# Kernel tuning notes

Hardware: AMD Instinct MI355X
Metric: run time of the kernel (lower is better)

## Reference

```python
import jax, jax.numpy as jnp
import numpy as np

N = 4096      # nodes
F = 512       # nfeat
D = 64        # nhid per head
H = 8         # nheads
C = 40        # nclass
ALPHA = 0.2   # leakyrelu slope
NEG = -1e9    # mask value (finite for bf16/fp16 safety; exp -> 0)
EDGE_P = 0.004


def setup_inputs() -> dict:
    key = jax.random.key(0)
    ks = jax.random.split(key, 8)
    x = jax.random.normal(ks[0], (N, F), jnp.float32)
    adj = jax.random.uniform(ks[1], (N, N)) < EDGE_P
    adj = adj | jnp.eye(N, dtype=bool)  # self-loops: every softmax row valid
    init = lambda k, shape, fan: jax.random.normal(k, shape, jnp.float32) / np.sqrt(fan)
    W1 = init(ks[2], (H, F, D), F)        # per-head tran.weight^T
    a1_src = init(ks[3], (H, D), D)       # att1 (j / source term)
    a1_dst = init(ks[4], (H, D), D)       # att2 (i / destination term)
    W2 = init(ks[5], (H * D, C), H * D)   # output head tran
    a2_src = init(ks[6], (C,), C)
    a2_dst = init(ks[7], (C,), C)
    return dict(x=x, adj=adj, W1=W1, a1_src=a1_src, a1_dst=a1_dst,
                W2=W2, a2_src=a2_src, a2_dst=a2_dst)


def reference(x, adj, W1, a1_src, a1_dst, W2, a2_src, a2_dst):
    # ---- layer 1: H heads in parallel (dropout = identity in eval) ----
    h = jnp.einsum('nf,hfd->hnd', x, W1)              # [H,N,D]
    si = jnp.einsum('hnd,hd->hn', h, a1_dst)          # att2(h): i term
    sj = jnp.einsum('hnd,hd->hn', h, a1_src)          # att1(h): j term
    e = jax.nn.leaky_relu(si[:, :, None] + sj[:, None, :], ALPHA)  # [H,N,N]
    e = jnp.where(adj[None], e, NEG)                  # mask non-edges
    p = jax.nn.softmax(e, axis=-1)                    # softmax over neighbors j
    out = jnp.einsum('hij,hjd->hid', p, h)            # [H,N,D]
    # torch.cat(heads, dim=1) -> [N, H*D] with heads contiguous
    x2 = jax.nn.elu(jnp.transpose(out, (1, 0, 2)).reshape(N, H * D))
    # ---- output attention head ----
    h2 = x2 @ W2                                      # [N,C]
    e2 = jax.nn.leaky_relu((h2 @ a2_dst)[:, None] + (h2 @ a2_src)[None, :], ALPHA)
    e2 = jnp.where(adj, e2, NEG)
    p2 = jax.nn.softmax(e2, axis=-1)
    return p2 @ h2                                    # [N,C]
```

## Files before the change

### kernel.cpp

```cpp
#include <hip/hip_runtime.h>

#define NN 4096
#define FF 512
#define DD 64
#define HH 8
#define CC 40
#define HD (HH * DD)
#define CP 64
#define MAXDEG 128
#define ALPHA 0.2f

#define L2BM 16
#define L2BK 32

typedef __attribute__((ext_vector_type(8))) short bf16x8;
typedef __attribute__((ext_vector_type(4))) float f32x4;

__device__ __forceinline__ float bf2f(unsigned short u) {
    union { unsigned int i; float f; } v;
    v.i = ((unsigned int)u) << 16;
    return v.f;
}

__device__ __forceinline__ unsigned short f2bf(float f) {
    union { float f; unsigned int u; } v;
    v.f = f;
    unsigned int r = v.u + 0x7fffu + ((v.u >> 16) & 1u);
    return (unsigned short)(r >> 16);
}

__device__ __forceinline__ float wave_sum(float v) {
    #pragma unroll
    for (int off = 32; off; off >>= 1) v += __shfl_xor(v, off, 64);
    return v;
}

__device__ __forceinline__ float wave_max(float v) {
    #pragma unroll
    for (int off = 32; off; off >>= 1) v = fmaxf(v, __shfl_xor(v, off, 64));
    return v;
}

__device__ __forceinline__ float read_f(const void* src, int i, int isBf16) {
    if (isBf16) return bf2f(((const unsigned short*)src)[i]);
    return ((const float*)src)[i];
}

__device__ __forceinline__ int sniff_x(const void* xraw, int tid, int* fS) {
    if (tid == 0) *fS = 1;
    __syncthreads();
    int bad = 0;
    const unsigned int* xw = (const unsigned int*)xraw;
    #pragma unroll
    for (int q = 0; q < 4; q++) {
        unsigned int w = xw[(tid & 255) * 4 + q];
        unsigned int e0 = (w >> 7) & 0xffu;
        unsigned int e1 = (w >> 23) & 0xffu;
        if (e0 >= 0x90u || e1 >= 0x90u) bad = 1;
    }
    if (bad) *fS = 0;
    __syncthreads();
    return *fS;
}

__global__ __launch_bounds__(256) void prep(const unsigned char* __restrict__ adj,
                                            const void* __restrict__ x,
                                            const void* __restrict__ W1,
                                            const void* __restrict__ W2,
                                            const void* __restrict__ a1s,
                                            const void* __restrict__ a1d,
                                            const void* __restrict__ a2s,
                                            const void* __restrict__ a2d,
                                            int* __restrict__ nbr,
                                            int* __restrict__ deg,
                                            unsigned short* __restrict__ W1bth,
                                            unsigned short* __restrict__ W1btl,
                                            float* __restrict__ W2p,
                                            float* __restrict__ a1sf,
                                            float* __restrict__ a1df,
                                            float* __restrict__ a2sf,
                                            float* __restrict__ a2df) {
    __shared__ int cnt;
    __shared__ int fS;
    int t = threadIdx.x;
    int blk = blockIdx.x;

    if (blk < NN) {
        if (t == 0) { cnt = 0; fS = 1; }
        __syncthreads();
        if (adj[(size_t)t * (NN + 1)] == 0) fS = 0;
        __syncthreads();
        int isByte = fS;
        int i = blk;
        if (isByte) {
            uint4 v = ((const uint4*)(adj + (size_t)i * NN))[t];
            unsigned int u[4] = { v.x, v.y, v.z, v.w };
            int base = t * 16;
            #pragma unroll
            for (int q = 0; q < 4; q++) {
                #pragma unroll
                for (int b = 0; b < 4; b++) {
                    if ((u[q] >> (8 * b)) & 0xffu) {
                        int p = atomicAdd(&cnt, 1);
                        if (p < MAXDEG) nbr[(size_t)i * MAXDEG + p] = base + q * 4 + b;
                    }
                }
            }
        } else {
            const int4* row = (const int4*)((const int*)adj + (size_t)i * NN);
            #pragma unroll
            for (int q = 0; q < 4; q++) {
                int idx4 = q * 256 + t;
                int4 v = row[idx4];
                int base = idx4 * 4;
                if (v.x) { int p = atomicAdd(&cnt, 1); if (p < MAXDEG) nbr[(size_t)i * MAXDEG + p] = base; }
                if (v.y) { int p = atomicAdd(&cnt, 1); if (p < MAXDEG) nbr[(size_t)i * MAXDEG + p] = base + 1; }
                if (v.z) { int p = atomicAdd(&cnt, 1); if (p < MAXDEG) nbr[(size_t)i * MAXDEG + p] = base + 2; }
                if (v.w) { int p = atomicAdd(&cnt, 1); if (p < MAXDEG) nbr[(size_t)i * MAXDEG + p] = base + 3; }
            }
        }
        __syncthreads();
        if (t == 0) deg[i] = min(cnt, MAXDEG);
        return;
    }

    int bf = sniff_x(x, t, &fS);

    if (blk < NN + 64) {
        int b = blk - NN;
        int ob = b * 4096 + t * 16;
        int row = ob >> 9;
        int f0 = ob & 511;
        int hd = row >> 6, d = row & 63;
        unsigned short hi[16], lo[16];
        #pragma unroll
        for (int q = 0; q < 16; q++) {
            float v = read_f(W1, (hd * FF + f0 + q) * DD + d, bf);
            unsigned short h16 = f2bf(v);
            hi[q] = h16;
            lo[q] = f2bf(v - bf2f(h16));
        }
        #pragma unroll
        for (int q = 0; q < 16; q++) {
            W1bth[(size_t)row * FF + f0 + q] = hi[q];
            W1btl[(size_t)row * FF + f0 + q] = lo[q];
        }
        return;
    }

    int i = (blk - NN - 64) * 256 + t;
    const int nW2p = HD * CP;
    const int nA1 = HD;
    if (i < nW2p) {
        int k = i / CP, c = i % CP;
        W2p[i] = (c < CC) ? read_f(W2, k * CC + c, bf) : 0.f;
        return;
    }
    i -= nW2p;
    if (i < nA1) { a1sf[i] = read_f(a1s, i, bf); return; }
    i -= nA1;
    if (i < nA1) { a1df[i] = read_f(a1d, i, bf); return; }
    i -= nA1;
    if (i < CC) { a2sf[i] = read_f(a2s, i, bf); return; }
    i -= CC;
    if (i < CC) { a2df[i] = read_f(a2d, i, bf); return; }
}

__global__ __launch_bounds__(256) void l1_gemm(const void* __restrict__ xraw,
                                               const unsigned short* __restrict__ W1bth,
                                               const unsigned short* __restrict__ W1btl,
                                               const float* __restrict__ a1sf,
                                               const float* __restrict__ a1df,
                                               unsigned short* __restrict__ hb,
                                               float* __restrict__ si,
                                               float* __restrict__ sj) {
    __shared__ __align__(16) unsigned short Ah[64][40];
    __shared__ __align__(16) unsigned short Al[64][40];
    __shared__ __align__(16) unsigned short Bh[64][40];
    __shared__ __align__(16) unsigned short Bl[64][40];
    __shared__ int fS;

    int bm = blockIdx.x, hd = blockIdx.y;
    int tid = threadIdx.x;
    int isBf16 = sniff_x(xraw, tid, &fS);

    int wave = tid >> 6, lane = tid & 63;
    int wm = wave >> 1, wn = wave & 1;
    int lr = lane & 15, lg = lane >> 4;
    int srow = tid >> 2;
    int sseg = (tid & 3) * 8;

    const unsigned short* wAp = W1bth + (size_t)(hd * 64 + srow) * FF + sseg;
    const unsigned short* wBp = W1btl + (size_t)(hd * 64 + srow) * FF + sseg;

    f32x4 acc[2][2];
    #pragma unroll
    for (int r = 0; r < 2; r++)
        #pragma unroll
        for (int c = 0; c < 2; c++) acc[r][c] = (f32x4){0.f, 0.f, 0.f, 0.f};

    if (isBf16) {
        const unsigned short* xp = (const unsigned short*)xraw
                                 + (size_t)(bm * 64 + srow) * FF + sseg;
        uint4 ra = *(const uint4*)xp;
        uint4 rb = *(const uint4*)wAp;
        for (int kk = 0; kk < FF; kk += 32) {
            __syncthreads();
            *(uint4*)&Ah[srow][sseg] = ra;
            *(uint4*)&Bh[srow][sseg] = rb;
            __syncthreads();
            int kn = (kk + 32 < FF) ? kk + 32 : kk;
            ra = *(const uint4*)(xp + kn);
            rb = *(const uint4*)(wAp + kn);
            bf16x8 a0 = *(const bf16x8*)&Ah[wm * 32 + lr][lg * 8];
            bf16x8 a1 = *(const bf16x8*)&Ah[wm * 32 + 16 + lr][lg * 8];
            bf16x8 b0 = *(const bf16x8*)&Bh[wn * 32 + lr][lg * 8];
            bf16x8 b1 = *(const bf16x8*)&Bh[wn * 32 + 16 + lr][lg * 8];
            acc[0][0] = __builtin_amdgcn_mfma_f32_16x16x32_bf16(a0, b0, acc[0][0], 0, 0, 0);
            acc[0][1] = __builtin_amdgcn_mfma_f32_16x16x32_bf16(a0, b1, acc[0][1], 0, 0, 0);
            acc[1][0] = __builtin_amdgcn_mfma_f32_16x16x32_bf16(a1, b0, acc[1][0], 0, 0, 0);
            acc[1][1] = __builtin_amdgcn_mfma_f32_16x16x32_bf16(a1, b1, acc[1][1], 0, 0, 0);
        }
    } else {
        const float* xp = (const float*)xraw + (size_t)(bm * 64 + srow) * FF + sseg;
        float4 ra0 = *(const float4*)xp;
        float4 ra1 = *(const float4*)(xp + 4);
        uint4 rbh = *(const uint4*)wAp;
        uint4 rbl = *(const uint4*)wBp;
        for (int kk = 0; kk < FF; kk += 32) {
            __syncthreads();
            union { unsigned short s[8]; uint4 v; } uh, ul;
            float fv[8] = { ra0.x, ra0.y, ra0.z, ra0.w, ra1.x, ra1.y, ra1.z, ra1.w };
            #pragma unroll
            for (int q = 0; q < 8; q++) {
                unsigned short h16 = f2bf(fv[q]);
                uh.s[q] = h16;
                ul.s[q] = f2bf(fv[q] - bf2f(h16));
            }
            *(uint4*)&Ah[srow][sseg] = uh.v;
            *(uint4*)&Al[srow][sseg] = ul.v;
            *(uint4*)&Bh[srow][sseg] = rbh;
            *(uint4*)&Bl[srow][sseg] = rbl;
            __syncthreads();
            int kn = (kk + 32 < FF) ? kk + 32 : kk;
            ra0 = *(const float4*)(xp + kn);
            ra1 = *(const float4*)(xp + kn + 4);
            rbh = *(const uint4*)(wAp + kn);
            rbl = *(const uint4*)(wBp + kn);

            bf16x8 a_h0 = *(const bf16x8*)&Ah[wm * 32 + lr][lg * 8];
            bf16x8 a_h1 = *(const bf16x8*)&Ah[wm * 32 + 16 + lr][lg * 8];
            bf16x8 a_l0 = *(const bf16x8*)&Al[wm * 32 + lr][lg * 8];
            bf16x8 a_l1 = *(const bf16x8*)&Al[wm * 32 + 16 + lr][lg * 8];
            bf16x8 b_h0 = *(const bf16x8*)&Bh[wn * 32 + lr][lg * 8];
            bf16x8 b_h1 = *(const bf16x8*)&Bh[wn * 32 + 16 + lr][lg * 8];
            bf16x8 b_l0 = *(const bf16x8*)&Bl[wn * 32 + lr][lg * 8];
            bf16x8 b_l1 = *(const bf16x8*)&Bl[wn * 32 + 16 + lr][lg * 8];

            acc[0][0] = __builtin_amdgcn_mfma_f32_16x16x32_bf16(a_h0, b_h0, acc[0][0], 0, 0, 0);
            acc[0][1] = __builtin_amdgcn_mfma_f32_16x16x32_bf16(a_h0, b_h1, acc[0][1], 0, 0, 0);
            acc[1][0] = __builtin_amdgcn_mfma_f32_16x16x32_bf16(a_h1, b_h0, acc[1][0], 0, 0, 0);
            acc[1][1] = __builtin_amdgcn_mfma_f32_16x16x32_bf16(a_h1, b_h1, acc[1][1], 0, 0, 0);
            acc[0][0] = __builtin_amdgcn_mfma_f32_16x16x32_bf16(a_h0, b_l0, acc[0][0], 0, 0, 0);
            acc[0][1] = __builtin_amdgcn_mfma_f32_16x16x32_bf16(a_h0, b_l1, acc[0][1], 0, 0, 0);
            acc[1][0] = __builtin_amdgcn_mfma_f32_16x16x32_bf16(a_h1, b_l0, acc[1][0], 0, 0, 0);
            acc[1][1] = __builtin_amdgcn_mfma_f32_16x16x32_bf16(a_h1, b_l1, acc[1][1], 0, 0, 0);
            acc[0][0] = __builtin_amdgcn_mfma_f32_16x16x32_bf16(a_l0, b_h0, acc[0][0], 0, 0, 0);
            acc[0][1] = __builtin_amdgcn_mfma_f32_16x16x32_bf16(a_l0, b_h1, acc[0][1], 0, 0, 0);
            acc[1][0] = __builtin_amdgcn_mfma_f32_16x16x32_bf16(a_l1, b_h0, acc[1][0], 0, 0, 0);
            acc[1][1] = __builtin_amdgcn_mfma_f32_16x16x32_bf16(a_l1, b_h1, acc[1][1], 0, 0, 0);
        }
    }

    float adv[2], asv[2];
    #pragma unroll
    for (int fc = 0; fc < 2; fc++) {
        adv[fc] = a1df[hd * DD + wn * 32 + fc * 16 + lr];
        asv[fc] = a1sf[hd * DD + wn * 32 + fc * 16 + lr];
    }
    float pdv[2][4], psv[2][4];
    #pragma unroll
    for (int fr = 0; fr < 2; fr++) {
        #pragma unroll
        for (int q = 0; q < 4; q++) {
            int row = bm * 64 + wm * 32 + fr * 16 + lg * 4 + q;
            int colb = hd * 64 + wn * 32;
            hb[(size_t)row * HD + colb + lr] = f2bf(acc[fr][0][q]);
            hb[(size_t)row * HD + colb + 16 + lr] = f2bf(acc[fr][1][q]);
            float pd = acc[fr][0][q] * adv[0] + acc[fr][1][q] * adv[1];
            float ps = acc[fr][0][q] * asv[0] + acc[fr][1][q] * asv[1];
            #pragma unroll
            for (int off = 1; off < 16; off <<= 1) {
                pd += __shfl_xor(pd, off, 64);
                ps += __shfl_xor(ps, off, 64);
            }
            pdv[fr][q] = pd;
            psv[fr][q] = ps;
        }
    }
    float* sred = (float*)&Ah[0][0];
    __syncthreads();
    if (wn == 0 && lr == 0) {
        #pragma unroll
        for (int fr = 0; fr < 2; fr++)
            #pragma unroll
            for (int q = 0; q < 4; q++) {
                int rl = wm * 32 + fr * 16 + lg * 4 + q;
                sred[rl * 2] = pdv[fr][q];
                sred[rl * 2 + 1] = psv[fr][q];
            }
    }
    __syncthreads();
    if (wn == 1 && lr == 0) {
        #pragma unroll
        for (int fr = 0; fr < 2; fr++)
            #pragma unroll
            for (int q = 0; q < 4; q++) {
                int rl = wm * 32 + fr * 16 + lg * 4 + q;
                int row = bm * 64 + rl;
                si[hd * NN + row] = sred[rl * 2] + pdv[fr][q];
                sj[hd * NN + row] = sred[rl * 2 + 1] + psv[fr][q];
            }
    }
}

__global__ __launch_bounds__(256) void l1_attn(const int* __restrict__ nbr,
                                               const int* __restrict__ deg,
                                               const unsigned short* __restrict__ hb,
                                               const float* __restrict__ si,
                                               const float* __restrict__ sj,
                                               float* __restrict__ x2) {
    int i = blockIdx.x;
    int tid = threadIdx.x;
    int wave = tid >> 6, lane = tid & 63;
    int d = deg[i];
    __shared__ int js[MAXDEG];
    __shared__ float wls[HH][MAXDEG];
    __shared__ float invs[HH];
    __shared__ __align__(16) float4 red[128];
    for (int k = tid; k < d; k += 256) js[k] = nbr[(size_t)i * MAXDEG + k];
    __syncthreads();

    int hd = wave * 2 + (lane >> 5);
    int l32 = lane & 31;
    float sii = si[hd * NN + i];
    const float* sjh = sj + (size_t)hd * NN;
    float m = -1e30f;
    for (int k = l32; k < d; k += 32) {
        float sc = sii + sjh[js[k]];
        sc = sc > 0.f ? sc : ALPHA * sc;
        wls[hd][k] = sc;
        m = fmaxf(m, sc);
    }
    #pragma unroll
    for (int off = 16; off; off >>= 1) m = fmaxf(m, __shfl_xor(m, off, 64));
    float s = 0.f;
    for (int k = l32; k < d; k += 32) {
        float e = expf(wls[hd][k] - m);
        wls[hd][k] = e;
        s += e;
    }
    #pragma unroll
    for (int off = 16; off; off >>= 1) s += __shfl_xor(s, off, 64);
    if (l32 == 0) invs[hd] = 1.f / fmaxf(s, 1e-30f);
    __syncthreads();

    const uint2* hu2 = (const uint2*)hb;
    int half = tid >> 7;
    int cq = tid & 127;
    const float* wl = wls[cq >> 4];
    float a0 = 0.f, a1 = 0.f, a2 = 0.f, a3 = 0.f;
    int kk = half;
    for (; kk + 4 <= d; kk += 4) {
        uint2 v0 = hu2[(size_t)js[kk] * 128 + cq];
        uint2 v1 = hu2[(size_t)js[kk + 2] * 128 + cq];
        float w0 = wl[kk], w1 = wl[kk + 2];
        a0 = fmaf(w0, bf2f((unsigned short)v0.x), a0);
        a1 = fmaf(w0, bf2f((unsigned short)(v0.x >> 16)), a1);
        a2 = fmaf(w0, bf2f((unsigned short)v0.y), a2);
        a3 = fmaf(w0, bf2f((unsigned short)(v0.y >> 16)), a3);
        a0 = fmaf(w1, bf2f((unsigned short)v1.x), a0);
        a1 = fmaf(w1, bf2f((unsigned short)(v1.x >> 16)), a1);
        a2 = fmaf(w1, bf2f((unsigned short)v1.y), a2);
        a3 = fmaf(w1, bf2f((unsigned short)(v1.y >> 16)), a3);
    }
    for (; kk < d; kk += 2) {
        uint2 v = hu2[(size_t)js[kk] * 128 + cq];
        float w = wl[kk];
        a0 = fmaf(w, bf2f((unsigned short)v.x), a0);
        a1 = fmaf(w, bf2f((unsigned short)(v.x >> 16)), a1);
        a2 = fmaf(w, bf2f((unsigned short)v.y), a2);
        a3 = fmaf(w, bf2f((unsigned short)(v.y >> 16)), a3);
    }
    if (half == 1) red[cq] = make_float4(a0, a1, a2, a3);
    __syncthreads();
    if (half == 0) {
        float4 r = red[cq];
        float inv = invs[cq >> 4];
        a0 = (a0 + r.x) * inv;
        a1 = (a1 + r.y) * inv;
        a2 = (a2 + r.z) * inv;
        a3 = (a3 + r.w) * inv;
        float4 o;
        o.x = a0 > 0.f ? a0 : expm1f(a0);
        o.y = a1 > 0.f ? a1 : expm1f(a1);
        o.z = a2 > 0.f ? a2 : expm1f(a2);
        o.w = a3 > 0.f ? a3 : expm1f(a3);
        *(float4*)(x2 + (size_t)i * HD + cq * 4) = o;
    }
}

__global__ __launch_bounds__(256) void l2_fused(const float* __restrict__ x2,
                                                const float* __restrict__ W2p,
                                                const float* __restrict__ a2sf,
                                                const float* __restrict__ a2df,
                                                float* __restrict__ h2,
                                                float* __restrict__ d1,
                                                float* __restrict__ d2) {
    __shared__ __align__(16) float As[L2BK][L2BM + 4];
    __shared__ float Bs[L2BK][CP + 1];
    int tid = threadIdx.x;
    int bm = blockIdx.x;
    int ar = tid >> 4;
    int ac2 = (tid & 15) * 2;
    int br = tid >> 3;
    int bc = (tid & 7) * 8;
    int c = tid & 63;
    int r0 = (tid >> 6) * 4;

    const float* Arow = x2 + (size_t)(bm * L2BM + ar) * FF;

    float acc0 = 0.f, acc1 = 0.f, acc2 = 0.f, acc3 = 0.f;

    float2 av = *(const float2*)(Arow + ac2);
    float4 bv0 = *(const float4*)(W2p + (size_t)br * CP + bc);
    float4 bv1 = *(const float4*)(W2p + (size_t)br * CP + bc + 4);

    for (int kk = 0; kk < FF; kk += L2BK) {
        __syncthreads();
        As[ac2 + 0][ar] = av.x;
        As[ac2 + 1][ar] = av.y;
        *(float4*)&Bs[br][bc] = bv0;
        *(float4*)&Bs[br][bc + 4] = bv1;
        __syncthreads();
        int kn = (kk + L2BK < FF) ? kk + L2BK : kk;
        av = *(const float2*)(Arow + kn + ac2);
        bv0 = *(const float4*)(W2p + (size_t)(kn + br) * CP + bc);
        bv1 = *(const float4*)(W2p + (size_t)(kn + br) * CP + bc + 4);
        #pragma unroll
        for (int k = 0; k < L2BK; k++) {
            float4 a = *(const float4*)&As[k][r0];
            float b = Bs[k][c];
            acc0 = fmaf(a.x, b, acc0);
            acc1 = fmaf(a.y, b, acc1);
            acc2 = fmaf(a.z, b, acc2);
            acc3 = fmaf(a.w, b, acc3);
        }
    }

    float accs[4] = { acc0, acc1, acc2, acc3 };
    float ad = (c < CC) ? a2df[c] : 0.f;
    float as = (c < CC) ? a2sf[c] : 0.f;
    #pragma unroll
    for (int q = 0; q < 4; q++) {
        int row = bm * L2BM + r0 + q;
        if (c < CC) h2[(size_t)row * CC + c] = accs[q];
        float pd = wave_sum(accs[q] * ad);
        float ps = wave_sum(accs[q] * as);
        if (c == 0) { d1[row] = pd; d2[row] = ps; }
    }
}

__global__ __launch_bounds__(256) void l2_attn(const int* __restrict__ nbr,
                                               const int* __restrict__ deg,
                                               const float* __restrict__ h2,
                                               const float* __restrict__ d1,
                                               const float* __restrict__ d2,
                                               float* __restrict__ out) {
    int w = threadIdx.x >> 6, lane = threadIdx.x & 63;
    int i = blockIdx.x * 4 + w;
    int d = deg[i];
    __shared__ int js[4][MAXDEG];
    __shared__ float wls[4][MAXDEG];
    for (int k = lane; k < d; k += 64) js[w][k] = nbr[(size_t)i * MAXDEG + k];

    float sii = d1[i];
    float m = -1e30f;
    for (int k = lane; k < d; k += 64) {
        float sc = sii + d2[js[w][k]];
        sc = sc > 0.f ? sc : ALPHA * sc;
        wls[w][k] = sc;
        m = fmaxf(m, sc);
    }
    m = wave_max(m);
    float s = 0.f;
    for (int k = lane; k < d; k += 64) {
        float e = expf(wls[w][k] - m);
        wls[w][k] = e;
        s += e;
    }
    s = fmaxf(wave_sum(s), 1e-30f);

    int c = lane;
    if (c < CC) {
        float acc = 0.f;
        int k = 0;
        for (; k + 4 <= d; k += 4) {
            float v0 = h2[(size_t)js[w][k] * CC + c];
            float v1 = h2[(size_t)js[w][k + 1] * CC + c];
            float v2 = h2[(size_t)js[w][k + 2] * CC + c];
            float v3 = h2[(size_t)js[w][k + 3] * CC + c];
            acc = fmaf(wls[w][k], v0, acc);
            acc = fmaf(wls[w][k + 1], v1, acc);
            acc = fmaf(wls[w][k + 2], v2, acc);
            acc = fmaf(wls[w][k + 3], v3, acc);
        }
        for (; k < d; k++)
            acc = fmaf(wls[w][k], h2[(size_t)js[w][k] * CC + c], acc);
        out[(size_t)i * CC + c] = acc / s;
    }
}

extern "C" void kernel_launch(void* const* d_in, const int* in_sizes, int n_in,
                              void* d_out, int out_size, void* d_ws, size_t ws_size,
                              hipStream_t stream) {
    const void* x   = d_in[0];
    const unsigned char* adj = (const unsigned char*)d_in[1];
    const void* W1  = d_in[2];
    const void* a1s = d_in[3];
    const void* a1d = d_in[4];
    const void* W2  = d_in[5];
    const void* a2s = d_in[6];
    const void* a2d = d_in[7];

    char* ws = (char*)d_ws;
    int*   nbr   = (int*)(ws + 0);
    int*   deg   = (int*)(ws + 2097152);
    float* si    = (float*)(ws + 2113536);
    float* sj    = (float*)(ws + 2244608);
    unsigned short* W1bth = (unsigned short*)(ws + 2375680);
    unsigned short* W1btl = (unsigned short*)(ws + 2899968);
    float* W2p   = (float*)(ws + 3424256);
    float* a1sf  = (float*)(ws + 3555328);
    float* a1df  = (float*)(ws + 3557376);
    float* a2sf  = (float*)(ws + 3559424);
    float* a2df  = (float*)(ws + 3559680);
    unsigned short* hb = (unsigned short*)(ws + 3559936);
    float* x2    = (float*)(ws + 7754240);
    float* h2    = (float*)(ws + 16142848);
    float* d1    = (float*)(ws + 16798208);
    float* d2    = (float*)(ws + 16814592);

    const int nSmall = HD * CP + 2 * HD + 2 * CC;
    const int prepGrid = NN + 64 + (nSmall + 255) / 256;
    hipLaunchKernelGGL(prep, dim3(prepGrid), dim3(256), 0, stream,
                       adj, x, W1, W2, a1s, a1d, a2s, a2d,
                       nbr, deg, W1bth, W1btl, W2p, a1sf, a1df, a2sf, a2df);

    hipLaunchKernelGGL(l1_gemm, dim3(NN / 64, HH), dim3(256), 0, stream,
                       x, W1bth, W1btl, a1sf, a1df, hb, si, sj);
    hipLaunchKernelGGL(l1_attn, dim3(NN), dim3(256), 0, stream,
                       nbr, deg, hb, si, sj, x2);
    hipLaunchKernelGGL(l2_fused, dim3(NN / L2BM), dim3(256), 0, stream,
                       x2, W2p, a2sf, a2df, h2, d1, d2);
    hipLaunchKernelGGL(l2_attn, dim3(NN / 4), dim3(256), 0, stream,
                       nbr, deg, h2, d1, d2, (float*)d_out);
}
```

Before: 168.0 us.

## Double-buffer L1 GEMM LDS, interleave si/sj per node, shrink L2 tile

New measurement: 171.1 us. Within noise of the previous version (+1.9%).

```diff
diff --git a/kernel.cpp b/kernel.cpp
--- a/kernel.cpp
+++ b/kernel.cpp
@@ -10,7 +10,7 @@
 #define MAXDEG 128
 #define ALPHA 0.2f
 
-#define L2BM 16
+#define L2BM 8
 #define L2BK 32
 
 typedef __attribute__((ext_vector_type(8))) short bf16x8;
@@ -172,12 +172,10 @@
                                                const float* __restrict__ a1sf,
                                                const float* __restrict__ a1df,
                                                unsigned short* __restrict__ hb,
-                                               float* __restrict__ si,
-                                               float* __restrict__ sj) {
-    __shared__ __align__(16) unsigned short Ah[64][40];
-    __shared__ __align__(16) unsigned short Al[64][40];
-    __shared__ __align__(16) unsigned short Bh[64][40];
-    __shared__ __align__(16) unsigned short Bl[64][40];
+                                               float* __restrict__ siv,
+                                               float* __restrict__ sjv) {
+    __shared__ __align__(16) unsigned short AhB[2][64][40];
+    __shared__ __align__(16) unsigned short BhB[2][64][40];
     __shared__ int fS;
 
     int bm = blockIdx.x, hd = blockIdx.y;
@@ -204,24 +202,29 @@
                                  + (size_t)(bm * 64 + srow) * FF + sseg;
         uint4 ra = *(const uint4*)xp;
         uint4 rb = *(const uint4*)wAp;
+        #pragma unroll 4
         for (int kk = 0; kk < FF; kk += 32) {
-            __syncthreads();
-            *(uint4*)&Ah[srow][sseg] = ra;
-            *(uint4*)&Bh[srow][sseg] = rb;
+            int p = (kk >> 5) & 1;
+            *(uint4*)&AhB[p][srow][sseg] = ra;
+            *(uint4*)&BhB[p][srow][sseg] = rb;
             __syncthreads();
             int kn = (kk + 32 < FF) ? kk + 32 : kk;
             ra = *(const uint4*)(xp + kn);
             rb = *(const uint4*)(wAp + kn);
-            bf16x8 a0 = *(const bf16x8*)&Ah[wm * 32 + lr][lg * 8];
-            bf16x8 a1 = *(const bf16x8*)&Ah[wm * 32 + 16 + lr][lg * 8];
-            bf16x8 b0 = *(const bf16x8*)&Bh[wn * 32 + lr][lg * 8];
-            bf16x8 b1 = *(const bf16x8*)&Bh[wn * 32 + 16 + lr][lg * 8];
+            bf16x8 a0 = *(const bf16x8*)&AhB[p][wm * 32 + lr][lg * 8];
+            bf16x8 a1 = *(const bf16x8*)&AhB[p][wm * 32 + 16 + lr][lg * 8];
+            bf16x8 b0 = *(const bf16x8*)&BhB[p][wn * 32 + lr][lg * 8];
+            bf16x8 b1 = *(const bf16x8*)&BhB[p][wn * 32 + 16 + lr][lg * 8];
             acc[0][0] = __builtin_amdgcn_mfma_f32_16x16x32_bf16(a0, b0, acc[0][0], 0, 0, 0);
             acc[0][1] = __builtin_amdgcn_mfma_f32_16x16x32_bf16(a0, b1, acc[0][1], 0, 0, 0);
             acc[1][0] = __builtin_amdgcn_mfma_f32_16x16x32_bf16(a1, b0, acc[1][0], 0, 0, 0);
             acc[1][1] = __builtin_amdgcn_mfma_f32_16x16x32_bf16(a1, b1, acc[1][1], 0, 0, 0);
         }
     } else {
+        unsigned short (*Ah)[40] = AhB[0];
+        unsigned short (*Al)[40] = AhB[1];
+        unsigned short (*Bh)[40] = BhB[0];
+        unsigned short (*Bl)[40] = BhB[1];
         const float* xp = (const float*)xraw + (size_t)(bm * 64 + srow) * FF + sseg;
         float4 ra0 = *(const float4*)xp;
         float4 ra1 = *(const float4*)(xp + 4);
@@ -298,7 +301,7 @@
             psv[fr][q] = ps;
         }
     }
-    float* sred = (float*)&Ah[0][0];
+    float* sred = (float*)&AhB[0][0][0];
     __syncthreads();
     if (wn == 0 && lr == 0) {
         #pragma unroll
@@ -318,8 +321,8 @@
             for (int q = 0; q < 4; q++) {
                 int rl = wm * 32 + fr * 16 + lg * 4 + q;
                 int row = bm * 64 + rl;
-                si[hd * NN + row] = sred[rl * 2] + pdv[fr][q];
-                sj[hd * NN + row] = sred[rl * 2 + 1] + psv[fr][q];
+                siv[(size_t)row * HH + hd] = sred[rl * 2] + pdv[fr][q];
+                sjv[(size_t)row * HH + hd] = sred[rl * 2 + 1] + psv[fr][q];
             }
     }
 }
@@ -327,8 +330,8 @@
 __global__ __launch_bounds__(256) void l1_attn(const int* __restrict__ nbr,
                                                const int* __restrict__ deg,
                                                const unsigned short* __restrict__ hb,
-                                               const float* __restrict__ si,
-                                               const float* __restrict__ sj,
+                                               const float* __restrict__ siv,
+                                               const float* __restrict__ sjv,
                                                float* __restrict__ x2) {
     int i = blockIdx.x;
     int tid = threadIdx.x;
@@ -343,11 +346,10 @@
 
     int hd = wave * 2 + (lane >> 5);
     int l32 = lane & 31;
-    float sii = si[hd * NN + i];
-    const float* sjh = sj + (size_t)hd * NN;
+    float sii = siv[(size_t)i * HH + hd];
     float m = -1e30f;
     for (int k = l32; k < d; k += 32) {
-        float sc = sii + sjh[js[k]];
+        float sc = sii + sjv[(size_t)js[k] * HH + hd];
         sc = sc > 0.f ? sc : ALPHA * sc;
         wls[hd][k] = sc;
         m = fmaxf(m, sc);
@@ -417,52 +419,48 @@
                                                 float* __restrict__ h2,
                                                 float* __restrict__ d1,
                                                 float* __restrict__ d2) {
-    __shared__ __align__(16) float As[L2BK][L2BM + 4];
+    __shared__ float As[L2BK][L2BM + 1];
     __shared__ float Bs[L2BK][CP + 1];
     int tid = threadIdx.x;
     int bm = blockIdx.x;
-    int ar = tid >> 4;
-    int ac2 = (tid & 15) * 2;
+    int ar = tid >> 5;
+    int ak = tid & 31;
     int br = tid >> 3;
     int bc = (tid & 7) * 8;
     int c = tid & 63;
-    int r0 = (tid >> 6) * 4;
+    int r0 = (tid >> 6) * 2;
 
     const float* Arow = x2 + (size_t)(bm * L2BM + ar) * FF;
 
-    float acc0 = 0.f, acc1 = 0.f, acc2 = 0.f, acc3 = 0.f;
-
-    float2 av = *(const float2*)(Arow + ac2);
+    float acc0 = 0.f, acc1 = 0.f;
+
+    float av = Arow[ak];
     float4 bv0 = *(const float4*)(W2p + (size_t)br * CP + bc);
     float4 bv1 = *(const float4*)(W2p + (size_t)br * CP + bc + 4);
 
     for (int kk = 0; kk < FF; kk += L2BK) {
         __syncthreads();
-        As[ac2 + 0][ar] = av.x;
-        As[ac2 + 1][ar] = av.y;
+        As[ak][ar] = av;
         *(float4*)&Bs[br][bc] = bv0;
         *(float4*)&Bs[br][bc + 4] = bv1;
         __syncthreads();
         int kn = (kk + L2BK < FF) ? kk + L2BK : kk;
-        av = *(const float2*)(Arow + kn + ac2);
+        av = Arow[kn + ak];
         bv0 = *(const float4*)(W2p + (size_t)(kn + br) * CP + bc);
         bv1 = *(const float4*)(W2p + (size_t)(kn + br) * CP + bc + 4);
         #pragma unroll
         for (int k = 0; k < L2BK; k++) {
-            float4 a = *(const float4*)&As[k][r0];
             float b = Bs[k][c];
-            acc0 = fmaf(a.x, b, acc0);
-            acc1 = fmaf(a.y, b, acc1);
-            acc2 = fmaf(a.z, b, acc2);
-            acc3 = fmaf(a.w, b, acc3);
-        }
-    }
-
-    float accs[4] = { acc0, acc1, acc2, acc3 };
+            acc0 = fmaf(As[k][r0], b, acc0);
+            acc1 = fmaf(As[k][r0 + 1], b, acc1);
+        }
+    }
+
+    float accs[2] = { acc0, acc1 };
     float ad = (c < CC) ? a2df[c] : 0.f;
     float as = (c < CC) ? a2sf[c] : 0.f;
     #pragma unroll
-    for (int q = 0; q < 4; q++) {
+    for (int q = 0; q < 2; q++) {
         int row = bm * L2BM + r0 + q;
         if (c < CC) h2[(size_t)row * CC + c] = accs[q];
         float pd = wave_sum(accs[q] * ad);
@@ -536,8 +534,8 @@
     char* ws = (char*)d_ws;
     int*   nbr   = (int*)(ws + 0);
     int*   deg   = (int*)(ws + 2097152);
-    float* si    = (float*)(ws + 2113536);
-    float* sj    = (float*)(ws + 2244608);
+    float* siv   = (float*)(ws + 2113536);
+    float* sjv   = (float*)(ws + 2244608);
     unsigned short* W1bth = (unsigned short*)(ws + 2375680);
     unsigned short* W1btl = (unsigned short*)(ws + 2899968);
     float* W2p   = (float*)(ws + 3424256);
@@ -553,14 +551,14 @@
 
     const int nSmall = HD * CP + 2 * HD + 2 * CC;
     const int prepGrid = NN + 64 + (nSmall + 255) / 256;
+
     hipLaunchKernelGGL(prep, dim3(prepGrid), dim3(256), 0, stream,
                        adj, x, W1, W2, a1s, a1d, a2s, a2d,
                        nbr, deg, W1bth, W1btl, W2p, a1sf, a1df, a2sf, a2df);
-
     hipLaunchKernelGGL(l1_gemm, dim3(NN / 64, HH), dim3(256), 0, stream,
-                       x, W1bth, W1btl, a1sf, a1df, hb, si, sj);
+                       x, W1bth, W1btl, a1sf, a1df, hb, siv, sjv);
     hipLaunchKernelGGL(l1_attn, dim3(NN), dim3(256), 0, stream,
-                       nbr, deg, hb, si, sj, x2);
+                       nbr, deg, hb, siv, sjv, x2);
     hipLaunchKernelGGL(l2_fused, dim3(NN / L2BM), dim3(256), 0, stream,
                        x2, W2p, a2sf, a2df, h2, d1, d2);
     hipLaunchKernelGGL(l2_attn, dim3(NN / 4), dim3(256), 0, stream,
```
